# Performance work log

Measured on AMD Instinct MI355X. Metric: run time of the kernel, lower is better.

Reference implementation:

```python
import jax, jax.numpy as jnp
import numpy as np

B, C_IN, H, W = 4, 64, 384, 384
C_OUT, KER, R = 64, 3, 4
N = B * H * W


def _conv(x, w):
    # NCHW conv, stride 1, SAME padding (ker//2 for odd kernels)
    return jax.lax.conv_general_dilated(
        x, w, window_strides=(1, 1), padding='SAME',
        dimension_numbers=('NCHW', 'OIHW', 'NCHW'))


def setup_inputs() -> dict:
    key = jax.random.key(0)
    kx, kp, k1, k2, k3 = jax.random.split(key, 5)
    x = jax.random.normal(kx, (B, C_IN, H, W), dtype=jnp.float32)
    # disjoint partition of all b*h*w pixel indices
    perm = jax.random.permutation(kp, N)
    mask_idx = perm[: N // 2].astype(jnp.int32)
    inv_mask_idx = perm[N // 2:].astype(jnp.int32)
    # weights, init per the torch module: std = sqrt(2 / (out_channels * kH*kW))
    std_high = np.sqrt(2.0 / (C_OUT * KER * KER)).astype(np.float32)
    std_low1 = np.sqrt(2.0 / ((C_OUT // R) * KER * KER)).astype(np.float32)
    std_low2 = np.sqrt(2.0 / (C_OUT * 1 * 1)).astype(np.float32)
    high_w = jax.random.normal(k1, (C_OUT, C_IN, KER, KER), dtype=jnp.float32) * std_high
    low1_w = jax.random.normal(k2, (C_OUT // R, C_IN, KER, KER), dtype=jnp.float32) * std_low1
    low2_w = jax.random.normal(k3, (C_OUT, C_OUT // R, 1, 1), dtype=jnp.float32) * std_low2
    return {"x": x, "high_w": high_w, "low1_w": low1_w, "low2_w": low2_w,
            "mask_idx": mask_idx, "inv_mask_idx": inv_mask_idx}


def reference(x, high_w, low1_w, low2_w, mask_idx, inv_mask_idx):
    # eval_forward: per-pixel routed conv (no bias on either path).
    # Pixels in mask_idx get the full 3x3 conv; pixels in inv_mask_idx get the
    # low-rank bottleneck path (3x3 conv to C/r, then 1x1 conv back to C).
    b, c, h, w = x.shape
    n = b * h * w
    high = _conv(x, high_w)                     # (b, cout, h, w)
    low = _conv(_conv(x, low1_w), low2_w)       # (b, cout, h, w)
    # flatten to pixel-major order matching torch's b*h*w flattening
    hf = high.transpose(0, 2, 3, 1).reshape(n, -1)  # (n, cout)
    lf = low.transpose(0, 2, 3, 1).reshape(n, -1)
    is_high = jnp.zeros((n,), dtype=bool).at[mask_idx].set(True)
    yf = jnp.where(is_high[:, None], hf, lf)
    return yf.reshape(b, h, w, -1).transpose(0, 3, 1, 2)
```

## Files before the change

### kernel.cpp

```cpp
#include <hip/hip_runtime.h>
#include <hip/hip_bf16.h>
#include <stdint.h>

typedef __attribute__((ext_vector_type(8))) short  short8;
typedef __attribute__((ext_vector_type(4))) float  float4_t;
typedef __attribute__((ext_vector_type(4))) int    int4_t;

constexpr int BB = 4, CIN = 64, COUT = 64, HH = 384, WW = 384;
constexpr int HWc  = HH * WW;
constexpr int NPIX = BB * HWc;
constexpr int TR = 8, TC = 32;
constexpr int SR = TR + 2, SC = TC + 2;
constexpr int NTASK = SR * 9 * 8;

__device__ __forceinline__ unsigned short f2bf(float f) {
    unsigned u = __builtin_bit_cast(unsigned, f);
    unsigned r = u + 0x7FFFu + ((u >> 16) & 1u);
    return (unsigned short)(r >> 16);
}

__global__ void k_flags(const int* __restrict__ mi, const int* __restrict__ ii,
                        unsigned char* __restrict__ flags, int half) {
    int i = blockIdx.x * blockDim.x + threadIdx.x;
    if (i < half) { flags[mi[i]] = 1; flags[ii[i]] = 0; }
}

__global__ void k_wpack(const float* __restrict__ hw_, const float* __restrict__ l1w,
                        const float* __restrict__ l2w,
                        unsigned short* __restrict__ Wp, unsigned short* __restrict__ Ap2) {
    int i = blockIdx.x * 256 + threadIdx.x;
    if (i < 18 * 5 * 64) {
        int lane = i & 63, tile = (i >> 6) % 5, chunk = i / 320;
        int tap = chunk >> 1, h = chunk & 1, ky = tap / 3, kx = tap % 3;
        int m = lane & 15, quad = lane >> 4;
        for (int j = 0; j < 8; j++) {
            int cin = h * 32 + quad * 8 + j;
            float wv;
            if (tile < 4) { int co = tile * 16 + m; wv = hw_[((co * 64 + cin) * 3 + ky) * 3 + kx]; }
            else          { wv = l1w[((m * 64 + cin) * 3 + ky) * 3 + kx]; }
            Wp[(size_t)i * 8 + j] = f2bf(wv);
        }
    }
    if (i < 4 * 64) {
        int lane = i & 63, tile = i >> 6;
        int m = lane & 15, quad = lane >> 4;
        for (int j = 0; j < 8; j++) {
            unsigned short v = 0;
            if (j < 4) { int c = quad * 4 + j; v = f2bf(l2w[(tile * 16 + m) * 16 + c]); }
            Ap2[(size_t)i * 8 + j] = v;
        }
    }
}

__global__ __launch_bounds__(256, 3) void k_main(
    const float* __restrict__ x,
    const unsigned short* __restrict__ Wp,
    const unsigned short* __restrict__ Ap2,
    const unsigned char* __restrict__ flags,
    float* __restrict__ out)
{
    __shared__ __align__(16) unsigned short X[SR * SC * 64];

    const int tid = threadIdx.x;
    const int x0  = blockIdx.x * TC;
    const int y0  = blockIdx.y * TR;
    const int b   = blockIdx.z;

    const float* xb = x + (size_t)b * CIN * HWc;
#pragma unroll 1
    for (int t = tid; t < NTASK; t += 256) {
        int g   = t % 9;
        int q   = (t / 9) & 7;
        int row = t / 72;
        int gy  = y0 + row - 1;
        int gx0 = x0 - 1 + g * 4;
        bool yok  = (unsigned)gy < (unsigned)HH;
        bool fast = yok && (gx0 >= 0) && (gx0 <= WW - 4);
        const float* xp = xb + (size_t)(q * 8) * HWc + gy * WW + gx0;
        float4_t v[8];
        if (fast) {
#pragma unroll
            for (int c = 0; c < 8; c++)
                v[c] = *(const float4_t*)(xp + (size_t)c * HWc);
        } else {
#pragma unroll
            for (int c = 0; c < 8; c++)
#pragma unroll
                for (int e = 0; e < 4; e++) {
                    bool ok = yok && ((unsigned)(gx0 + e) < (unsigned)WW);
                    v[c][e] = ok ? xp[(size_t)c * HWc + e] : 0.f;
                }
        }
#pragma unroll
        for (int e = 0; e < 4; e++) {
            int col = g * 4 + e;
            if (col < SC) {
                unsigned pk[4];
#pragma unroll
                for (int jj = 0; jj < 4; jj++)
                    pk[jj] = (unsigned)f2bf(v[2 * jj][e]) | ((unsigned)f2bf(v[2 * jj + 1][e]) << 16);
                int blk = q ^ (col & 7);
                *(int4_t*)&X[(row * SC + col) * 64 + blk * 8] = *(int4_t*)pk;
            }
        }
    }
    __syncthreads();

    const int lane = tid & 63;
    const int w    = tid >> 6;
    const int n16  = lane & 15;
    const int quad = lane >> 4;

    float4_t acc[5][4];
#pragma unroll
    for (int t = 0; t < 5; t++)
#pragma unroll
        for (int f = 0; f < 4; f++) acc[t][f] = (float4_t)0.0f;

    const int4_t* wp4 = (const int4_t*)Wp;
    short8 a_cur[5], a_nxt[5];
#pragma unroll
    for (int t = 0; t < 5; t++)
        a_cur[t] = __builtin_bit_cast(short8, wp4[t * 64 + lane]);

#pragma unroll 1
    for (int chunk = 0; chunk < 18; chunk++) {
        if (chunk < 17) {
#pragma unroll
            for (int t = 0; t < 5; t++)
                a_nxt[t] = __builtin_bit_cast(short8, wp4[((chunk + 1) * 5 + t) * 64 + lane]);
        }
        const int tap = chunk >> 1, h = chunk & 1;
        const int ky = tap / 3, kx = tap % 3;
        short8 bf[4];
#pragma unroll
        for (int f = 0; f < 4; f++) {
            int r  = 2 * w + (f >> 1);
            int ch = f & 1;
            int xh  = ch * 16 + n16 + kx;
            int blk = (h * 4 + quad) ^ (xh & 7);
            bf[f] = __builtin_bit_cast(short8,
                    *(const int4_t*)&X[((r + ky) * SC + xh) * 64 + blk * 8]);
        }
#pragma unroll
        for (int f = 0; f < 4; f++)
#pragma unroll
            for (int t = 0; t < 5; t++)
                acc[t][f] = __builtin_amdgcn_mfma_f32_16x16x32_bf16(a_cur[t], bf[f], acc[t][f], 0, 0, 0);
#pragma unroll
        for (int t = 0; t < 5; t++) a_cur[t] = a_nxt[t];
    }

    short8 a2[4];
    const int4_t* ap4 = (const int4_t*)Ap2;
#pragma unroll
    for (int t = 0; t < 4; t++)
        a2[t] = __builtin_bit_cast(short8, ap4[t * 64 + lane]);

#pragma unroll
    for (int f = 0; f < 4; f++) {
        int r  = 2 * w + (f >> 1);
        int ch = f & 1;
        float4_t m4 = acc[4][f];
        short8 bfrag;
#pragma unroll
        for (int j = 0; j < 8; j++)
            bfrag[j] = (j < 4) ? (short)f2bf(m4[j]) : (short)0;

        int gy = y0 + r, gx = x0 + ch * 16 + n16;
        bool hiF = flags[b * HWc + gy * WW + gx] != 0;
        float* ob = out + (size_t)b * COUT * HWc + gy * WW + gx;
#pragma unroll
        for (int t = 0; t < 4; t++) {
            float4_t low = __builtin_amdgcn_mfma_f32_16x16x32_bf16(a2[t], bfrag, (float4_t)0.0f, 0, 0, 0);
            float4_t hi = acc[t][f];
#pragma unroll
            for (int i = 0; i < 4; i++) {
                int co = t * 16 + quad * 4 + i;
                ob[(size_t)co * HWc] = hiF ? hi[i] : low[i];
            }
        }
    }
}

extern "C" void kernel_launch(void* const* d_in, const int* in_sizes, int n_in,
                              void* d_out, int out_size, void* d_ws, size_t ws_size,
                              hipStream_t stream) {
    const float* x   = (const float*)d_in[0];
    const float* hw_ = (const float*)d_in[1];
    const float* l1w = (const float*)d_in[2];
    const float* l2w = (const float*)d_in[3];
    const int*   mi  = (const int*)d_in[4];
    const int*   ii  = (const int*)d_in[5];
    float*       out = (float*)d_out;

    unsigned char*  flags = (unsigned char*)d_ws;
    size_t off = (NPIX + 15) & ~(size_t)15;
    unsigned short* Wp    = (unsigned short*)((char*)d_ws + off); off += 18 * 5 * 64 * 8 * 2;
    unsigned short* Ap2   = (unsigned short*)((char*)d_ws + off);

    const int half = NPIX / 2;
    k_flags<<<(half + 255) / 256, 256, 0, stream>>>(mi, ii, flags, half);
    k_wpack<<<(18 * 5 * 64 + 255) / 256, 256, 0, stream>>>(hw_, l1w, l2w, Wp, Ap2);
    k_main<<<dim3(WW / TC, HH / TR, BB), 256, 0, stream>>>(x, Wp, Ap2, flags, out);
}
```

Before: 328.5 us.

## Fuse prep kernels, swizzle blocks across XCDs, align halo loads, use packed bf16 cvt

```diff
diff --git a/kernel.cpp b/kernel.cpp
--- a/kernel.cpp
+++ b/kernel.cpp
@@ -11,7 +11,12 @@
 constexpr int NPIX = BB * HWc;
 constexpr int TR = 8, TC = 32;
 constexpr int SR = TR + 2, SC = TC + 2;
-constexpr int NTASK = SR * 9 * 8;
+constexpr int NG = 10;
+constexpr int NTASK = SR * NG * 8;
+constexpr int NXTILE = WW / TC;
+constexpr int NYTILE = HH / TR;
+constexpr int NBLK  = NXTILE * NYTILE * BB;
+constexpr int XCD_CHUNK = NBLK / 8;
 
 __device__ __forceinline__ unsigned short f2bf(float f) {
     unsigned u = __builtin_bit_cast(unsigned, f);
@@ -19,16 +24,19 @@
     return (unsigned short)(r >> 16);
 }
 
-__global__ void k_flags(const int* __restrict__ mi, const int* __restrict__ ii,
-                        unsigned char* __restrict__ flags, int half) {
-    int i = blockIdx.x * blockDim.x + threadIdx.x;
+__device__ __forceinline__ unsigned cvtpk(float lo, float hi) {
+    unsigned r;
+    asm("v_cvt_pk_bf16_f32 %0, %1, %2" : "=v"(r) : "v"(lo), "v"(hi));
+    return r;
+}
+
+__global__ void k_prep(const int* __restrict__ mi, const int* __restrict__ ii,
+                       unsigned char* __restrict__ flags, int half,
+                       const float* __restrict__ hw_, const float* __restrict__ l1w,
+                       const float* __restrict__ l2w,
+                       unsigned short* __restrict__ Wp, unsigned short* __restrict__ Ap2) {
+    int i = blockIdx.x * 256 + threadIdx.x;
     if (i < half) { flags[mi[i]] = 1; flags[ii[i]] = 0; }
-}
-
-__global__ void k_wpack(const float* __restrict__ hw_, const float* __restrict__ l1w,
-                        const float* __restrict__ l2w,
-                        unsigned short* __restrict__ Wp, unsigned short* __restrict__ Ap2) {
-    int i = blockIdx.x * 256 + threadIdx.x;
     if (i < 18 * 5 * 64) {
         int lane = i & 63, tile = (i >> 6) % 5, chunk = i / 320;
         int tap = chunk >> 1, h = chunk & 1, ky = tap / 3, kx = tap % 3;
@@ -62,18 +70,32 @@
     __shared__ __align__(16) unsigned short X[SR * SC * 64];
 
     const int tid = threadIdx.x;
-    const int x0  = blockIdx.x * TC;
-    const int y0  = blockIdx.y * TR;
-    const int b   = blockIdx.z;
+
+    const int lin = blockIdx.x;
+    const int des = (lin & 7) * XCD_CHUNK + (lin >> 3);
+    const int xt  = des % NXTILE;
+    const int rst = des / NXTILE;
+    const int yt  = rst % NYTILE;
+    const int b   = rst / NYTILE;
+    const int x0  = xt * TC;
+    const int y0  = yt * TR;
+
+    const int lane = tid & 63;
+
+    const int4_t* wp4 = (const int4_t*)Wp;
+    short8 a_cur[5], a_nxt[5];
+#pragma unroll
+    for (int t = 0; t < 5; t++)
+        a_cur[t] = __builtin_bit_cast(short8, wp4[t * 64 + lane]);
 
     const float* xb = x + (size_t)b * CIN * HWc;
 #pragma unroll 1
     for (int t = tid; t < NTASK; t += 256) {
-        int g   = t % 9;
-        int q   = (t / 9) & 7;
-        int row = t / 72;
+        int g   = t % NG;
+        int q   = (t / NG) & 7;
+        int row = t / (NG * 8);
         int gy  = y0 + row - 1;
-        int gx0 = x0 - 1 + g * 4;
+        int gx0 = x0 - 4 + g * 4;
         bool yok  = (unsigned)gy < (unsigned)HH;
         bool fast = yok && (gx0 >= 0) && (gx0 <= WW - 4);
         const float* xp = xb + (size_t)(q * 8) * HWc + gy * WW + gx0;
@@ -93,20 +115,19 @@
         }
 #pragma unroll
         for (int e = 0; e < 4; e++) {
-            int col = g * 4 + e;
-            if (col < SC) {
-                unsigned pk[4];
+            int col = g * 4 + e - 3;
+            if ((unsigned)col < (unsigned)SC) {
+                int4_t pk;
 #pragma unroll
                 for (int jj = 0; jj < 4; jj++)
-                    pk[jj] = (unsigned)f2bf(v[2 * jj][e]) | ((unsigned)f2bf(v[2 * jj + 1][e]) << 16);
+                    pk[jj] = (int)cvtpk(v[2 * jj][e], v[2 * jj + 1][e]);
                 int blk = q ^ (col & 7);
-                *(int4_t*)&X[(row * SC + col) * 64 + blk * 8] = *(int4_t*)pk;
+                *(int4_t*)&X[(row * SC + col) * 64 + blk * 8] = pk;
             }
         }
     }
     __syncthreads();
 
-    const int lane = tid & 63;
     const int w    = tid >> 6;
     const int n16  = lane & 15;
     const int quad = lane >> 4;
@@ -116,12 +137,6 @@
     for (int t = 0; t < 5; t++)
 #pragma unroll
         for (int f = 0; f < 4; f++) acc[t][f] = (float4_t)0.0f;
-
-    const int4_t* wp4 = (const int4_t*)Wp;
-    short8 a_cur[5], a_nxt[5];
-#pragma unroll
-    for (int t = 0; t < 5; t++)
-        a_cur[t] = __builtin_bit_cast(short8, wp4[t * 64 + lane]);
 
 #pragma unroll 1
     for (int chunk = 0; chunk < 18; chunk++) {
@@ -162,10 +177,12 @@
         int r  = 2 * w + (f >> 1);
         int ch = f & 1;
         float4_t m4 = acc[4][f];
-        short8 bfrag;
-#pragma unroll
-        for (int j = 0; j < 8; j++)
-            bfrag[j] = (j < 4) ? (short)f2bf(m4[j]) : (short)0;
+        int4_t bi;
+        bi[0] = (int)cvtpk(m4[0], m4[1]);
+        bi[1] = (int)cvtpk(m4[2], m4[3]);
+        bi[2] = 0;
+        bi[3] = 0;
+        short8 bfrag = __builtin_bit_cast(short8, bi);
 
         int gy = y0 + r, gx = x0 + ch * 16 + n16;
         bool hiF = flags[b * HWc + gy * WW + gx] != 0;
@@ -200,7 +217,6 @@
     unsigned short* Ap2   = (unsigned short*)((char*)d_ws + off);
 
     const int half = NPIX / 2;
-    k_flags<<<(half + 255) / 256, 256, 0, stream>>>(mi, ii, flags, half);
-    k_wpack<<<(18 * 5 * 64 + 255) / 256, 256, 0, stream>>>(hw_, l1w, l2w, Wp, Ap2);
-    k_main<<<dim3(WW / TC, HH / TR, BB), 256, 0, stream>>>(x, Wp, Ap2, flags, out);
-}
+    k_prep<<<(half + 255) / 256, 256, 0, stream>>>(mi, ii, flags, half, hw_, l1w, l2w, Wp, Ap2);
+    k_main<<<NBLK, 256, 0, stream>>>(x, Wp, Ap2, flags, out);
+}
```

Measured after the change: 316.0 us. 1.04x faster.
